# Performance work log

Hardware: AMD Instinct MI355X
Metric: run time of the kernel (lower is better)

The kernel has to match this reference:

```python
import jax, jax.numpy as jnp
import numpy as np


def setup_inputs() -> dict:
    key = jax.random.key(0)
    k_x, k_pos, k_val, k_temp = jax.random.split(key, 4)
    B, T, D, N = 8, 2048, 512, 4096
    x = jax.random.normal(k_x, (B, T, D), dtype=jnp.float32)
    # module init: positions ~ N(0,1)*0.5, values ~ N(0,1)*0.02
    positions = jax.random.normal(k_pos, (N, D), dtype=jnp.float32) * 0.5
    values = jax.random.normal(k_val, (N, D), dtype=jnp.float32) * 0.02
    # 'trained' temperatures ~ U[4,6] so the RBF kernel does not underflow at D=512
    temperature = 4.0 + 2.0 * jax.random.uniform(k_temp, (N,), dtype=jnp.float32)
    # neuron_scale buffer at late-tide level (MAX_SCALE = 0.8)
    neuron_scale = jnp.full((N,), 0.8, dtype=jnp.float32)
    return {"x": x, "positions": positions, "values": values,
            "temperature": temperature, "neuron_scale": neuron_scale}


def reference(x, positions, values, temperature, neuron_scale):
    B, T, D = x.shape
    x_flat = x.reshape(-1, D)                                  # [M, D], M = B*T
    x_sq = jnp.sum(x_flat * x_flat, axis=-1, keepdims=True)    # [M, 1]
    p_sq = jnp.sum(positions * positions, axis=-1)             # [N]
    cross = x_flat @ positions.T                               # [M, N] GEMM
    dists = jnp.sqrt(jnp.maximum(x_sq + p_sq[None, :] - 2.0 * cross, 0.0))
    effective_temp = (jnp.abs(temperature) + 0.1) * neuron_scale  # [N]
    weights = jnp.exp(-dists / effective_temp[None, :])        # [M, N]
    weights = weights / (jnp.sum(weights, axis=-1, keepdims=True) + 1e-8)
    out = weights @ values                                     # [M, D] GEMM
    return out.reshape(B, T, D)
```

## Files before the change

### kernel.cpp

```cpp
#include <hip/hip_runtime.h>
#include <hip/hip_bf16.h>

typedef __attribute__((ext_vector_type(8))) short short8;
typedef __attribute__((ext_vector_type(4))) float f32x4;
typedef __attribute__((ext_vector_type(4))) unsigned short u16x4;

__device__ __forceinline__ unsigned short f2bf(float f) {
  union { float f; unsigned u; } v; v.f = f;
  unsigned r = v.u + 0x7fffu + ((v.u >> 16) & 1u);
  return (unsigned short)(r >> 16);
}

template <int EPI>
__global__ __launch_bounds__(512, 4) void rbf_gemm(
    const unsigned short* __restrict__ A, const unsigned short* __restrict__ Bt,
    int Ncols, int K,
    const float* __restrict__ xsq, const float* __restrict__ psq,
    const float* __restrict__ rtemp, unsigned short* __restrict__ Wout,
    float* __restrict__ part, int Mtot, const float* __restrict__ denin,
    float* __restrict__ outp, int row0, int ldOut) {
  constexpr int HALF = 8192;
  __shared__ __align__(16) unsigned short smem[16384];

  const int t = threadIdx.x;
  const int lane = t & 63, wid = t >> 6;
  const int wr = wid >> 1, wc = wid & 1;
  const int lr = lane & 15, lg = lane >> 4;

  const int nb = Ncols >> 7;
  const int nwg = gridDim.x;
  int swz = blockIdx.x;
  if ((nwg & 7) == 0) {
    int cpx = nwg >> 3;
    swz = (swz & 7) * cpx + (swz >> 3);
  }
  const int bm = swz / nb, bn = swz - bm * nb;

  const unsigned short* Ab = A + (size_t)bm * 128 * K;
  const unsigned short* Bb = Bt + (size_t)bn * 128 * K;

  const int sr = t >> 2, sc = t & 3;
  const int scs = sc ^ ((sr >> 1) & 3);
  const unsigned short* gA = Ab + (size_t)sr * K + scs * 8;
  const unsigned short* gB = Bb + (size_t)sr * K + scs * 8;
  const int dbase = wid << 9;

  int offA[2], offB[4];
#pragma unroll
  for (int mi = 0; mi < 2; ++mi) {
    const int ar = wr * 32 + mi * 16 + lr;
    offA[mi] = ar * 32 + ((lg ^ ((ar >> 1) & 3)) << 3);
  }
#pragma unroll
  for (int ni = 0; ni < 4; ++ni) {
    const int br = wc * 64 + ni * 16 + lr;
    offB[ni] = 4096 + br * 32 + ((lg ^ ((br >> 1) & 3)) << 3);
  }

  f32x4 acc[2][4];
#pragma unroll
  for (int i = 0; i < 2; ++i)
#pragma unroll
    for (int j = 0; j < 4; ++j) acc[i][j] = (f32x4){0.f, 0.f, 0.f, 0.f};

#define STAGE(koff, boff)                                                          \
  do {                                                                             \
    __builtin_amdgcn_global_load_lds(                                              \
        (const __attribute__((address_space(1))) void*)(gA + (koff)),              \
        (__attribute__((address_space(3))) void*)(smem + (boff) + dbase), 16, 0, 0); \
    __builtin_amdgcn_global_load_lds(                                              \
        (const __attribute__((address_space(1))) void*)(gB + (koff)),              \
        (__attribute__((address_space(3))) void*)(smem + (boff) + 4096 + dbase), 16, 0, 0); \
  } while (0)

  STAGE(0, 0);
  __syncthreads();
  unsigned boff = 0;
  const int nsteps = K >> 5;
  for (int s = 0; s < nsteps; ++s) {
    if (s + 1 < nsteps) STAGE((s + 1) << 5, boff ^ HALF);
    const unsigned short* sb = smem + boff;
    short8 af[2], bf[4];
#pragma unroll
    for (int mi = 0; mi < 2; ++mi) af[mi] = *(const short8*)&sb[offA[mi]];
#pragma unroll
    for (int ni = 0; ni < 4; ++ni) bf[ni] = *(const short8*)&sb[offB[ni]];
#pragma unroll
    for (int mi = 0; mi < 2; ++mi)
#pragma unroll
      for (int ni = 0; ni < 4; ++ni)
        acc[mi][ni] = __builtin_amdgcn_mfma_f32_16x16x32_bf16(af[mi], bf[ni],
                                                              acc[mi][ni], 0, 0, 0);
    __syncthreads();
    boff ^= HALF;
  }
#undef STAGE

  if (EPI == 0) {
    float xv[2][4];
#pragma unroll
    for (int mi = 0; mi < 2; ++mi)
#pragma unroll
      for (int j = 0; j < 4; ++j)
        xv[mi][j] = xsq[row0 + bm * 128 + wr * 32 + mi * 16 + lg * 4 + j];

    float rs[2][4];
#pragma unroll
    for (int mi = 0; mi < 2; ++mi)
#pragma unroll
      for (int j = 0; j < 4; ++j) rs[mi][j] = 0.f;

#pragma unroll
    for (int ni = 0; ni < 4; ++ni) {
      const int lcol = wc * 64 + ni * 16 + lr;
      const int col = bn * 128 + lcol;
      const float ps = psq[col];
      const float rt = rtemp[col];
      const int h = lcol >> 3;
#pragma unroll
      for (int mi = 0; mi < 2; ++mi) {
#pragma unroll
        for (int j = 0; j < 4; ++j) {
          const int lrow = wr * 32 + mi * 16 + lg * 4 + j;
          float d2 = xv[mi][j] + ps - 2.0f * acc[mi][ni][j];
          float dist = __builtin_amdgcn_sqrtf(fmaxf(d2, 0.0f));
          float wgt = __expf(-dist * rt);
          smem[lrow * 128 + ((h ^ (lrow & 15)) << 3) + (lcol & 7)] = f2bf(wgt);
          rs[mi][j] += wgt;
        }
      }
    }
    __syncthreads();
#pragma unroll
    for (int i = 0; i < 4; ++i) {
      const int id = i * 512 + t;
      const int r = id >> 4, h = id & 15;
      short8 v = *(const short8*)&smem[r * 128 + ((h ^ (r & 15)) << 3)];
      *(short8*)&Wout[(size_t)(bm * 128 + r) * ldOut + bn * 128 + h * 8] = v;
    }
    float* slice = part + (size_t)((bn << 1) | wc) * Mtot;
#pragma unroll
    for (int mi = 0; mi < 2; ++mi)
#pragma unroll
      for (int j = 0; j < 4; ++j) {
        float v = rs[mi][j];
        v += __shfl_xor(v, 1);
        v += __shfl_xor(v, 2);
        v += __shfl_xor(v, 4);
        v += __shfl_xor(v, 8);
        if (lr == 0) {
          const int grow = row0 + bm * 128 + wr * 32 + mi * 16 + lg * 4 + j;
          slice[grow] = v;
        }
      }
  } else {
#pragma unroll
    for (int mi = 0; mi < 2; ++mi) {
#pragma unroll
      for (int j = 0; j < 4; ++j) {
        const int grow = row0 + bm * 128 + wr * 32 + mi * 16 + lg * 4 + j;
        const float rd = 1.0f / (denin[grow] + 1e-8f);
#pragma unroll
        for (int ni = 0; ni < 4; ++ni) {
          const int col = bn * 128 + wc * 64 + ni * 16 + lr;
          outp[(size_t)grow * ldOut + col] = acc[mi][ni][j] * rd;
        }
      }
    }
  }
}

__global__ void reduce_denom(const float* __restrict__ part, float* __restrict__ denom,
                             int Mtot, int row0, int S) {
  const int m = row0 + blockIdx.x * 128 + threadIdx.x;
  float s = 0.f;
  for (int i = 0; i < S; ++i) s += part[(size_t)i * Mtot + m];
  denom[m] = s;
}

__global__ void prep_rows(const float* __restrict__ in, unsigned short* __restrict__ outb,
                          float* __restrict__ sq, int D) {
  const int row = blockIdx.x;
  const int t = threadIdx.x;
  const float4 v = ((const float4*)(in + (size_t)row * D))[t];
  u16x4 o = {f2bf(v.x), f2bf(v.y), f2bf(v.z), f2bf(v.w)};
  *(u16x4*)(outb + (size_t)row * D + t * 4) = o;
  float s = v.x * v.x + v.y * v.y + v.z * v.z + v.w * v.w;
  for (int off = 32; off; off >>= 1) s += __shfl_xor(s, off);
  __shared__ float ws[16];
  if ((t & 63) == 0) ws[t >> 6] = s;
  __syncthreads();
  if (t == 0) {
    float tot = 0.f;
    const int nw = blockDim.x >> 6;
    for (int i = 0; i < nw; ++i) tot += ws[i];
    sq[row] = tot;
  }
}

__global__ void prep_scale(const float* __restrict__ tmp, const float* __restrict__ sc,
                           float* __restrict__ rtemp, int N) {
  const int i = blockIdx.x * blockDim.x + threadIdx.x;
  if (i < N) rtemp[i] = 1.0f / ((fabsf(tmp[i]) + 0.1f) * sc[i]);
}

__global__ void prep_vT(const float* __restrict__ vals, unsigned short* __restrict__ vT,
                        int N, int D) {
  __shared__ float tile[32][33];
  const int nt = blockIdx.x, dt = blockIdx.y;
  const int tx = threadIdx.x, ty = threadIdx.y;
#pragma unroll
  for (int i = 0; i < 4; ++i) {
    int r = nt * 32 + ty + i * 8;
    tile[ty + i * 8][tx] = vals[(size_t)r * D + dt * 32 + tx];
  }
  __syncthreads();
#pragma unroll
  for (int i = 0; i < 4; ++i) {
    int d = dt * 32 + ty + i * 8;
    vT[(size_t)d * N + nt * 32 + tx] = f2bf(tile[tx][ty + i * 8]);
  }
}

extern "C" void kernel_launch(void* const* d_in, const int* in_sizes, int n_in,
                              void* d_out, int out_size, void* d_ws, size_t ws_size,
                              hipStream_t stream) {
  const float* x = (const float*)d_in[0];
  const float* pos = (const float*)d_in[1];
  const float* vals = (const float*)d_in[2];
  const float* temp = (const float*)d_in[3];
  const float* nsc = (const float*)d_in[4];
  float* out = (float*)d_out;

  const int N = in_sizes[3];
  const int D = in_sizes[1] / N;
  const int M = in_sizes[0] / D;
  const int S = 2 * (N / 128);

  char* ws = (char*)d_ws;
  size_t off = 0;
  auto alloc = [&](size_t bytes) {
    void* p = ws + off;
    off = (off + bytes + 255) & ~(size_t)255;
    return p;
  };
  unsigned short* xb = (unsigned short*)alloc((size_t)M * D * 2);
  unsigned short* pb = (unsigned short*)alloc((size_t)N * D * 2);
  unsigned short* vT = (unsigned short*)alloc((size_t)D * N * 2);
  float* xsq = (float*)alloc((size_t)M * 4);
  float* psq = (float*)alloc((size_t)N * 4);
  float* rtemp = (float*)alloc((size_t)N * 4);
  float* denom = (float*)alloc((size_t)M * 4);
  float* part = (float*)alloc((size_t)S * M * 4);

  size_t avail = ws_size > off ? ws_size - off : 0;
  long long mc_ll = (long long)(avail / ((size_t)N * 2));
  int Mc = (int)((mc_ll / 128) * 128);
  if (Mc > M) Mc = M;
  if (Mc < 128) Mc = 128;
  unsigned short* W = (unsigned short*)alloc((size_t)Mc * N * 2);

  prep_rows<<<M, D / 4, 0, stream>>>(x, xb, xsq, D);
  prep_rows<<<N, D / 4, 0, stream>>>(pos, pb, psq, D);
  prep_scale<<<(N + 255) / 256, 256, 0, stream>>>(temp, nsc, rtemp, N);
  dim3 tg(N / 32, D / 32);
  prep_vT<<<tg, dim3(32, 8), 0, stream>>>(vals, vT, N, D);

  for (int row0 = 0; row0 < M; row0 += Mc) {
    const int mc = (M - row0) < Mc ? (M - row0) : Mc;
    const int g1 = (mc / 128) * (N / 128);
    rbf_gemm<0><<<g1, 512, 0, stream>>>(xb + (size_t)row0 * D, pb, N, D,
                                        xsq, psq, rtemp, W, part, M,
                                        nullptr, nullptr, row0, N);
    reduce_denom<<<mc / 128, 128, 0, stream>>>(part, denom, M, row0, S);
    const int g2 = (mc / 128) * (D / 128);
    rbf_gemm<1><<<g2, 512, 0, stream>>>(W, vT, D, N,
                                        nullptr, nullptr, nullptr, nullptr,
                                        part, M, denom, out, row0, D);
  }
}
```

Measured before the change: 226.9 us.

## Double K-tile depth to 64 per stage and use nontemporal epilogue stores

The GEMM main loop now stages a 64-wide K slice per iteration instead of 32. This halves the number of barriers and loop iterations and issues twice as many MFMAs between syncs. The LDS layout becomes 64-element rows with an 8-way XOR swizzle, the load mapping is reworked, and LDS use doubles to 64KB per block, which may reduce occupancy. Epilogue stores of weights, partial sums and output are made nontemporal to avoid polluting cache.

Result: no change. 230.0 us (+1.4%).

```diff
diff --git a/kernel.cpp b/kernel.cpp
--- a/kernel.cpp
+++ b/kernel.cpp
@@ -19,8 +19,8 @@
     const float* __restrict__ rtemp, unsigned short* __restrict__ Wout,
     float* __restrict__ part, int Mtot, const float* __restrict__ denin,
     float* __restrict__ outp, int row0, int ldOut) {
-  constexpr int HALF = 8192;
-  __shared__ __align__(16) unsigned short smem[16384];
+  constexpr int HALF = 16384;
+  __shared__ __align__(16) unsigned short smem[2 * HALF];
 
   const int t = threadIdx.x;
   const int lane = t & 63, wid = t >> 6;
@@ -39,22 +39,32 @@
   const unsigned short* Ab = A + (size_t)bm * 128 * K;
   const unsigned short* Bb = Bt + (size_t)bn * 128 * K;
 
-  const int sr = t >> 2, sc = t & 3;
-  const int scs = sc ^ ((sr >> 1) & 3);
-  const unsigned short* gA = Ab + (size_t)sr * K + scs * 8;
-  const unsigned short* gB = Bb + (size_t)sr * K + scs * 8;
+  const unsigned short* gA[2];
+  const unsigned short* gB[2];
+#pragma unroll
+  for (int i = 0; i < 2; ++i) {
+    const int idx = i * 512 + t;
+    const int r = idx >> 3, c = idx & 7;
+    const int cs = c ^ (r & 7);
+    gA[i] = Ab + (size_t)r * K + cs * 8;
+    gB[i] = Bb + (size_t)r * K + cs * 8;
+  }
   const int dbase = wid << 9;
 
-  int offA[2], offB[4];
+  int offA[2][2], offB[4][2];
 #pragma unroll
   for (int mi = 0; mi < 2; ++mi) {
     const int ar = wr * 32 + mi * 16 + lr;
-    offA[mi] = ar * 32 + ((lg ^ ((ar >> 1) & 3)) << 3);
+#pragma unroll
+    for (int ks = 0; ks < 2; ++ks)
+      offA[mi][ks] = ar * 64 + (((ks << 2) | lg) ^ (ar & 7)) * 8;
   }
 #pragma unroll
   for (int ni = 0; ni < 4; ++ni) {
     const int br = wc * 64 + ni * 16 + lr;
-    offB[ni] = 4096 + br * 32 + ((lg ^ ((br >> 1) & 3)) << 3);
+#pragma unroll
+    for (int ks = 0; ks < 2; ++ks)
+      offB[ni][ks] = 8192 + br * 64 + (((ks << 2) | lg) ^ (br & 7)) * 8;
   }
 
   f32x4 acc[2][4];
@@ -63,34 +73,45 @@
 #pragma unroll
     for (int j = 0; j < 4; ++j) acc[i][j] = (f32x4){0.f, 0.f, 0.f, 0.f};
 
-#define STAGE(koff, boff)                                                          \
-  do {                                                                             \
-    __builtin_amdgcn_global_load_lds(                                              \
-        (const __attribute__((address_space(1))) void*)(gA + (koff)),              \
-        (__attribute__((address_space(3))) void*)(smem + (boff) + dbase), 16, 0, 0); \
-    __builtin_amdgcn_global_load_lds(                                              \
-        (const __attribute__((address_space(1))) void*)(gB + (koff)),              \
-        (__attribute__((address_space(3))) void*)(smem + (boff) + 4096 + dbase), 16, 0, 0); \
+#define STAGE(koff, boff)                                                            \
+  do {                                                                               \
+    _Pragma("unroll")                                                                \
+    for (int i = 0; i < 2; ++i) {                                                    \
+      __builtin_amdgcn_global_load_lds(                                              \
+          (const __attribute__((address_space(1))) void*)(gA[i] + (koff)),           \
+          (__attribute__((address_space(3))) void*)(smem + (boff) + i * 4096 + dbase), \
+          16, 0, 0);                                                                 \
+      __builtin_amdgcn_global_load_lds(                                              \
+          (const __attribute__((address_space(1))) void*)(gB[i] + (koff)),           \
+          (__attribute__((address_space(3))) void*)(smem + (boff) + 8192 + i * 4096 + dbase), \
+          16, 0, 0);                                                                 \
+    }                                                                                \
   } while (0)
 
   STAGE(0, 0);
   __syncthreads();
   unsigned boff = 0;
-  const int nsteps = K >> 5;
+  const int nsteps = K >> 6;
   for (int s = 0; s < nsteps; ++s) {
-    if (s + 1 < nsteps) STAGE((s + 1) << 5, boff ^ HALF);
+    if (s + 1 < nsteps) STAGE((s + 1) << 6, boff ^ HALF);
     const unsigned short* sb = smem + boff;
-    short8 af[2], bf[4];
-#pragma unroll
-    for (int mi = 0; mi < 2; ++mi) af[mi] = *(const short8*)&sb[offA[mi]];
-#pragma unroll
-    for (int ni = 0; ni < 4; ++ni) bf[ni] = *(const short8*)&sb[offB[ni]];
+    short8 af[2][2], bf[4][2];
 #pragma unroll
     for (int mi = 0; mi < 2; ++mi)
 #pragma unroll
-      for (int ni = 0; ni < 4; ++ni)
-        acc[mi][ni] = __builtin_amdgcn_mfma_f32_16x16x32_bf16(af[mi], bf[ni],
-                                                              acc[mi][ni], 0, 0, 0);
+      for (int ks = 0; ks < 2; ++ks) af[mi][ks] = *(const short8*)&sb[offA[mi][ks]];
+#pragma unroll
+    for (int ni = 0; ni < 4; ++ni)
+#pragma unroll
+      for (int ks = 0; ks < 2; ++ks) bf[ni][ks] = *(const short8*)&sb[offB[ni][ks]];
+#pragma unroll
+    for (int ks = 0; ks < 2; ++ks)
+#pragma unroll
+      for (int mi = 0; mi < 2; ++mi)
+#pragma unroll
+        for (int ni = 0; ni < 4; ++ni)
+          acc[mi][ni] = __builtin_amdgcn_mfma_f32_16x16x32_bf16(af[mi][ks], bf[ni][ks],
+                                                                acc[mi][ni], 0, 0, 0);
     __syncthreads();
     boff ^= HALF;
   }
@@ -136,7 +157,8 @@
       const int id = i * 512 + t;
       const int r = id >> 4, h = id & 15;
       short8 v = *(const short8*)&smem[r * 128 + ((h ^ (r & 15)) << 3)];
-      *(short8*)&Wout[(size_t)(bm * 128 + r) * ldOut + bn * 128 + h * 8] = v;
+      __builtin_nontemporal_store(v,
+          (short8*)&Wout[(size_t)(bm * 128 + r) * ldOut + bn * 128 + h * 8]);
     }
     float* slice = part + (size_t)((bn << 1) | wc) * Mtot;
 #pragma unroll
@@ -150,7 +172,7 @@
         v += __shfl_xor(v, 8);
         if (lr == 0) {
           const int grow = row0 + bm * 128 + wr * 32 + mi * 16 + lg * 4 + j;
-          slice[grow] = v;
+          __builtin_nontemporal_store(v, &slice[grow]);
         }
       }
   } else {
@@ -163,7 +185,8 @@
 #pragma unroll
         for (int ni = 0; ni < 4; ++ni) {
           const int col = bn * 128 + wc * 64 + ni * 16 + lr;
-          outp[(size_t)grow * ldOut + col] = acc[mi][ni][j] * rd;
+          __builtin_nontemporal_store(acc[mi][ni][j] * rd,
+                                      &outp[(size_t)grow * ldOut + col]);
         }
       }
     }
```

## Enlarge GEMM tiles to 256x256 / 128x256 with K=64 steps and LDS-staged epilogues

Applied to the files above, without the earlier changes.

Reworks the templated bf16 MFMA GEMM to use larger block tiles: 256x256 for the distance/weight GEMM and 128x256 for the weights-times-values GEMM. Each main-loop step now covers 64 K elements (two MFMA sub-steps), and the LDS swizzle is rewritten for 64-element rows. Both epilogues are staged through LDS so global stores are coalesced and nontemporal. The aim is more data reuse per loaded tile, fewer barriers per unit of work and better-coalesced output writes. The cost is a 128KB LDS buffer and launch_bounds(512,2), which lowers occupancy, and fewer workgroups in the second GEMM.

After: 233.1 us. 1.03x slower.

```diff
diff --git a/kernel.cpp b/kernel.cpp
--- a/kernel.cpp
+++ b/kernel.cpp
@@ -11,23 +11,26 @@
   return (unsigned short)(r >> 16);
 }
 
-template <int EPI>
-__global__ __launch_bounds__(512, 4) void rbf_gemm(
+template <int EPI, int MI>
+__global__ __launch_bounds__(512, 2) void rbf_gemm(
     const unsigned short* __restrict__ A, const unsigned short* __restrict__ Bt,
     int Ncols, int K,
     const float* __restrict__ xsq, const float* __restrict__ psq,
     const float* __restrict__ rtemp, unsigned short* __restrict__ Wout,
     float* __restrict__ part, int Mtot, const float* __restrict__ denin,
     float* __restrict__ outp, int row0, int ldOut) {
-  constexpr int HALF = 8192;
-  __shared__ __align__(16) unsigned short smem[16384];
+  constexpr int BM = MI * 32;
+  constexpr int AITERS = BM / 64;
+  constexpr int ASZ = BM * 64;
+  constexpr int HALF = ASZ + 16384;
+  __shared__ __align__(16) unsigned short smem[65536];
 
   const int t = threadIdx.x;
   const int lane = t & 63, wid = t >> 6;
-  const int wr = wid >> 1, wc = wid & 1;
+  const int wm = wid >> 2, wn = wid & 3;
   const int lr = lane & 15, lg = lane >> 4;
 
-  const int nb = Ncols >> 7;
+  const int nb = Ncols >> 8;
   const int nwg = gridDim.x;
   int swz = blockIdx.x;
   if ((nwg & 7) == 0) {
@@ -36,136 +39,156 @@
   }
   const int bm = swz / nb, bn = swz - bm * nb;
 
-  const unsigned short* Ab = A + (size_t)bm * 128 * K;
-  const unsigned short* Bb = Bt + (size_t)bn * 128 * K;
-
-  const int sr = t >> 2, sc = t & 3;
-  const int scs = sc ^ ((sr >> 1) & 3);
-  const unsigned short* gA = Ab + (size_t)sr * K + scs * 8;
-  const unsigned short* gB = Bb + (size_t)sr * K + scs * 8;
-  const int dbase = wid << 9;
-
-  int offA[2], offB[4];
-#pragma unroll
-  for (int mi = 0; mi < 2; ++mi) {
-    const int ar = wr * 32 + mi * 16 + lr;
-    offA[mi] = ar * 32 + ((lg ^ ((ar >> 1) & 3)) << 3);
+  const unsigned short* Ab = A + (size_t)bm * BM * K;
+  const unsigned short* Bb = Bt + (size_t)bn * 256 * K;
+
+  const unsigned short* gA[AITERS];
+  const unsigned short* gB[4];
+#pragma unroll
+  for (int i = 0; i < AITERS; ++i) {
+    const int idx = i * 512 + t;
+    const int r = idx >> 3, c = idx & 7;
+    gA[i] = Ab + (size_t)r * K + ((c ^ (r & 7)) << 3);
+  }
+#pragma unroll
+  for (int i = 0; i < 4; ++i) {
+    const int idx = i * 512 + t;
+    const int r = idx >> 3, c = idx & 7;
+    gB[i] = Bb + (size_t)r * K + ((c ^ (r & 7)) << 3);
+  }
+  const int dwave = wid << 9;
+
+  int offA[MI][2], offB[4][2];
+#pragma unroll
+  for (int mi = 0; mi < MI; ++mi) {
+    const int ar = wm * (MI * 16) + mi * 16 + lr;
+#pragma unroll
+    for (int ks = 0; ks < 2; ++ks)
+      offA[mi][ks] = ar * 64 + ((((ks << 2) | lg) ^ (ar & 7)) << 3);
   }
 #pragma unroll
   for (int ni = 0; ni < 4; ++ni) {
-    const int br = wc * 64 + ni * 16 + lr;
-    offB[ni] = 4096 + br * 32 + ((lg ^ ((br >> 1) & 3)) << 3);
-  }
-
-  f32x4 acc[2][4];
-#pragma unroll
-  for (int i = 0; i < 2; ++i)
+    const int br = wn * 64 + ni * 16 + lr;
+#pragma unroll
+    for (int ks = 0; ks < 2; ++ks)
+      offB[ni][ks] = ASZ + br * 64 + ((((ks << 2) | lg) ^ (br & 7)) << 3);
+  }
+
+  f32x4 acc[MI][4];
+#pragma unroll
+  for (int i = 0; i < MI; ++i)
 #pragma unroll
     for (int j = 0; j < 4; ++j) acc[i][j] = (f32x4){0.f, 0.f, 0.f, 0.f};
 
-#define STAGE(koff, boff)                                                          \
-  do {                                                                             \
-    __builtin_amdgcn_global_load_lds(                                              \
-        (const __attribute__((address_space(1))) void*)(gA + (koff)),              \
-        (__attribute__((address_space(3))) void*)(smem + (boff) + dbase), 16, 0, 0); \
-    __builtin_amdgcn_global_load_lds(                                              \
-        (const __attribute__((address_space(1))) void*)(gB + (koff)),              \
-        (__attribute__((address_space(3))) void*)(smem + (boff) + 4096 + dbase), 16, 0, 0); \
+#define STAGE(koff, boff)                                                              \
+  do {                                                                                 \
+    _Pragma("unroll")                                                                  \
+    for (int i = 0; i < AITERS; ++i)                                                   \
+      __builtin_amdgcn_global_load_lds(                                                \
+          (const __attribute__((address_space(1))) void*)(gA[i] + (koff)),             \
+          (__attribute__((address_space(3))) void*)(smem + (boff) + i * 4096 + dwave), \
+          16, 0, 0);                                                                   \
+    _Pragma("unroll")                                                                  \
+    for (int i = 0; i < 4; ++i)                                                        \
+      __builtin_amdgcn_global_load_lds(                                                \
+          (const __attribute__((address_space(1))) void*)(gB[i] + (koff)),             \
+          (__attribute__((address_space(3))) void*)(smem + (boff) + ASZ + i * 4096 + dwave), \
+          16, 0, 0);                                                                   \
   } while (0)
 
   STAGE(0, 0);
   __syncthreads();
-  unsigned boff = 0;
-  const int nsteps = K >> 5;
+  unsigned buf = 0;
+  const int nsteps = K >> 6;
   for (int s = 0; s < nsteps; ++s) {
-    if (s + 1 < nsteps) STAGE((s + 1) << 5, boff ^ HALF);
-    const unsigned short* sb = smem + boff;
-    short8 af[2], bf[4];
-#pragma unroll
-    for (int mi = 0; mi < 2; ++mi) af[mi] = *(const short8*)&sb[offA[mi]];
-#pragma unroll
-    for (int ni = 0; ni < 4; ++ni) bf[ni] = *(const short8*)&sb[offB[ni]];
-#pragma unroll
-    for (int mi = 0; mi < 2; ++mi)
-#pragma unroll
-      for (int ni = 0; ni < 4; ++ni)
-        acc[mi][ni] = __builtin_amdgcn_mfma_f32_16x16x32_bf16(af[mi], bf[ni],
-                                                              acc[mi][ni], 0, 0, 0);
+    if (s + 1 < nsteps) STAGE((s + 1) << 6, buf ^ HALF);
+    const unsigned short* sb = smem + buf;
+#pragma unroll
+    for (int ks = 0; ks < 2; ++ks) {
+      short8 af[MI], bf[4];
+#pragma unroll
+      for (int mi = 0; mi < MI; ++mi) af[mi] = *(const short8*)&sb[offA[mi][ks]];
+#pragma unroll
+      for (int ni = 0; ni < 4; ++ni) bf[ni] = *(const short8*)&sb[offB[ni][ks]];
+#pragma unroll
+      for (int mi = 0; mi < MI; ++mi)
+#pragma unroll
+        for (int ni = 0; ni < 4; ++ni)
+          acc[mi][ni] = __builtin_amdgcn_mfma_f32_16x16x32_bf16(af[mi], bf[ni],
+                                                                acc[mi][ni], 0, 0, 0);
+    }
     __syncthreads();
-    boff ^= HALF;
+    buf ^= HALF;
   }
 #undef STAGE
 
   if (EPI == 0) {
-    float xv[2][4];
-#pragma unroll
-    for (int mi = 0; mi < 2; ++mi)
-#pragma unroll
-      for (int j = 0; j < 4; ++j)
-        xv[mi][j] = xsq[row0 + bm * 128 + wr * 32 + mi * 16 + lg * 4 + j];
-
-    float rs[2][4];
-#pragma unroll
-    for (int mi = 0; mi < 2; ++mi)
-#pragma unroll
-      for (int j = 0; j < 4; ++j) rs[mi][j] = 0.f;
-
+    float ps[4], rt[4];
 #pragma unroll
     for (int ni = 0; ni < 4; ++ni) {
-      const int lcol = wc * 64 + ni * 16 + lr;
-      const int col = bn * 128 + lcol;
-      const float ps = psq[col];
-      const float rt = rtemp[col];
-      const int h = lcol >> 3;
-#pragma unroll
-      for (int mi = 0; mi < 2; ++mi) {
-#pragma unroll
-        for (int j = 0; j < 4; ++j) {
-          const int lrow = wr * 32 + mi * 16 + lg * 4 + j;
-          float d2 = xv[mi][j] + ps - 2.0f * acc[mi][ni][j];
+      const int col = bn * 256 + wn * 64 + ni * 16 + lr;
+      ps[ni] = psq[col];
+      rt[ni] = rtemp[col];
+    }
+    float* slice = part + (size_t)(bn * 4 + wn) * Mtot;
+#pragma unroll
+    for (int mi = 0; mi < MI; ++mi) {
+#pragma unroll
+      for (int j = 0; j < 4; ++j) {
+        const int lrow = wm * (MI * 16) + mi * 16 + lg * 4 + j;
+        const int grow = row0 + bm * BM + lrow;
+        const float xq = xsq[grow];
+        float rsv = 0.f;
+#pragma unroll
+        for (int ni = 0; ni < 4; ++ni) {
+          const int lcol = wn * 64 + ni * 16 + lr;
+          float d2 = xq + ps[ni] - 2.0f * acc[mi][ni][j];
           float dist = __builtin_amdgcn_sqrtf(fmaxf(d2, 0.0f));
-          float wgt = __expf(-dist * rt);
-          smem[lrow * 128 + ((h ^ (lrow & 15)) << 3) + (lcol & 7)] = f2bf(wgt);
-          rs[mi][j] += wgt;
+          float w = __expf(-dist * rt[ni]);
+          smem[lrow * 256 + (((lcol >> 3) ^ (lrow & 7)) << 3) + (lcol & 7)] = f2bf(w);
+          rsv += w;
+        }
+        rsv += __shfl_xor(rsv, 1);
+        rsv += __shfl_xor(rsv, 2);
+        rsv += __shfl_xor(rsv, 4);
+        rsv += __shfl_xor(rsv, 8);
+        if (lr == 0) slice[grow] = rsv;
+      }
+    }
+    __syncthreads();
+#pragma unroll
+    for (int i = 0; i < BM / 16; ++i) {
+      const int id = i * 512 + t;
+      const int r = id >> 5, h = id & 31;
+      short8 v = *(const short8*)&smem[r * 256 + ((h ^ (r & 7)) << 3)];
+      __builtin_nontemporal_store(v,
+          (short8*)&Wout[(size_t)(bm * BM + r) * ldOut + bn * 256 + h * 8]);
+    }
+  } else {
+    float* smemf = (float*)smem;
+#pragma unroll
+    for (int mi = 0; mi < MI; ++mi)
+#pragma unroll
+      for (int j = 0; j < 4; ++j) {
+        const int lrow = wm * (MI * 16) + mi * 16 + lg * 4 + j;
+#pragma unroll
+        for (int ni = 0; ni < 4; ++ni) {
+          const int lcol = wn * 64 + ni * 16 + lr;
+          smemf[lrow * 256 + (((lcol >> 2) ^ (lrow & 7)) << 2) + (lcol & 3)] =
+              acc[mi][ni][j];
         }
       }
-    }
     __syncthreads();
 #pragma unroll
-    for (int i = 0; i < 4; ++i) {
+    for (int i = 0; i < BM / 8; ++i) {
       const int id = i * 512 + t;
-      const int r = id >> 4, h = id & 15;
-      short8 v = *(const short8*)&smem[r * 128 + ((h ^ (r & 15)) << 3)];
-      *(short8*)&Wout[(size_t)(bm * 128 + r) * ldOut + bn * 128 + h * 8] = v;
-    }
-    float* slice = part + (size_t)((bn << 1) | wc) * Mtot;
-#pragma unroll
-    for (int mi = 0; mi < 2; ++mi)
-#pragma unroll
-      for (int j = 0; j < 4; ++j) {
-        float v = rs[mi][j];
-        v += __shfl_xor(v, 1);
-        v += __shfl_xor(v, 2);
-        v += __shfl_xor(v, 4);
-        v += __shfl_xor(v, 8);
-        if (lr == 0) {
-          const int grow = row0 + bm * 128 + wr * 32 + mi * 16 + lg * 4 + j;
-          slice[grow] = v;
-        }
-      }
-  } else {
-#pragma unroll
-    for (int mi = 0; mi < 2; ++mi) {
-#pragma unroll
-      for (int j = 0; j < 4; ++j) {
-        const int grow = row0 + bm * 128 + wr * 32 + mi * 16 + lg * 4 + j;
-        const float rd = 1.0f / (denin[grow] + 1e-8f);
-#pragma unroll
-        for (int ni = 0; ni < 4; ++ni) {
-          const int col = bn * 128 + wc * 64 + ni * 16 + lr;
-          outp[(size_t)grow * ldOut + col] = acc[mi][ni][j] * rd;
-        }
-      }
+      const int r = id >> 6, h = id & 63;
+      const int grow = row0 + bm * BM + r;
+      const float rd = 1.0f / (denin[grow] + 1e-8f);
+      f32x4 v = *(const f32x4*)&smemf[r * 256 + ((h ^ (r & 7)) << 2)];
+      v *= rd;
+      __builtin_nontemporal_store(v,
+          (f32x4*)&outp[(size_t)grow * ldOut + bn * 256 + h * 4]);
     }
   }
 }
@@ -235,7 +258,7 @@
   const int N = in_sizes[3];
   const int D = in_sizes[1] / N;
   const int M = in_sizes[0] / D;
-  const int S = 2 * (N / 128);
+  const int S = 4 * (N / 256);
 
   char* ws = (char*)d_ws;
   size_t off = 0;
@@ -255,9 +278,9 @@
 
   size_t avail = ws_size > off ? ws_size - off : 0;
   long long mc_ll = (long long)(avail / ((size_t)N * 2));
-  int Mc = (int)((mc_ll / 128) * 128);
+  int Mc = (int)((mc_ll / 256) * 256);
   if (Mc > M) Mc = M;
-  if (Mc < 128) Mc = 128;
+  if (Mc < 256) Mc = 256;
   unsigned short* W = (unsigned short*)alloc((size_t)Mc * N * 2);
 
   prep_rows<<<M, D / 4, 0, stream>>>(x, xb, xsq, D);
@@ -268,14 +291,14 @@
 
   for (int row0 = 0; row0 < M; row0 += Mc) {
     const int mc = (M - row0) < Mc ? (M - row0) : Mc;
-    const int g1 = (mc / 128) * (N / 128);
-    rbf_gemm<0><<<g1, 512, 0, stream>>>(xb + (size_t)row0 * D, pb, N, D,
-                                        xsq, psq, rtemp, W, part, M,
-                                        nullptr, nullptr, row0, N);
+    const int g1 = (mc / 256) * (N / 256);
+    rbf_gemm<0, 8><<<g1, 512, 0, stream>>>(xb + (size_t)row0 * D, pb, N, D,
+                                           xsq, psq, rtemp, W, part, M,
+                                           nullptr, nullptr, row0, N);
     reduce_denom<<<mc / 128, 128, 0, stream>>>(part, denom, M, row0, S);
-    const int g2 = (mc / 128) * (D / 128);
-    rbf_gemm<1><<<g2, 512, 0, stream>>>(W, vT, D, N,
-                                        nullptr, nullptr, nullptr, nullptr,
-                                        part, M, denom, out, row0, D);
-  }
-}
+    const int g2 = (mc / 128) * (D / 256);
+    rbf_gemm<1, 4><<<g2, 512, 0, stream>>>(W, vT, D, N,
+                                           nullptr, nullptr, nullptr, nullptr,
+                                           part, M, denom, out, row0, D);
+  }
+}
```
